# Kernel optimization log

Measured on AMD Instinct MI355X. Metric: run time of the kernel, lower is better.

The kernel has to match this reference:

```python
import jax, jax.numpy as jnp
import numpy as np

NUM_HEADS = 16

def _apply_rope(x, cos, sin):
    # x: (B, H, T, D); cos/sin: (T, D//2)
    B, H, T, D = x.shape
    xr = x.reshape(B, H, T, D // 2, 2)
    x0, x1 = xr[..., 0], xr[..., 1]
    c = cos[None, None, :, :]
    s = sin[None, None, :, :]
    out = jnp.stack([x0 * c - x1 * s, x0 * s + x1 * c], axis=-1)
    return out.reshape(B, H, T, D)


def setup_inputs() -> dict:
    key = jax.random.key(0)
    k1, k2, k3 = jax.random.split(key, 3)
    B, T, C = 2, 2048, 1024
    D = C // NUM_HEADS
    x = jax.random.normal(k1, (B, T, C), dtype=jnp.float32)
    qkv_w = jax.random.normal(k2, (3 * C, C), dtype=jnp.float32) * (C ** -0.5)
    proj_w = jax.random.normal(k3, (C, C), dtype=jnp.float32) * (C ** -0.5)
    # standard RoPE frequency table (theta = 10000)
    inv_freq = 1.0 / (10000.0 ** (jnp.arange(0, D, 2, dtype=jnp.float32) / D))  # (D/2,)
    angles = jnp.arange(T, dtype=jnp.float32)[:, None] * inv_freq[None, :]      # (T, D/2)
    return {
        "x": x,
        "freqs_cos": jnp.cos(angles),
        "freqs_sin": jnp.sin(angles),
        "qkv_w": qkv_w,
        "proj_w": proj_w,
    }


def reference(x, freqs_cos, freqs_sin, qkv_w, proj_w):
    B, T, C = x.shape
    H = NUM_HEADS
    D = C // H
    qkv = x @ qkv_w.T                                  # (B, T, 3C)
    q, k, v = jnp.split(qkv, 3, axis=-1)
    q = q.reshape(B, T, H, D).transpose(0, 2, 1, 3)    # (B, H, T, D)
    k = k.reshape(B, T, H, D).transpose(0, 2, 1, 3)
    v = v.reshape(B, T, H, D).transpose(0, 2, 1, 3)
    q = _apply_rope(q, freqs_cos, freqs_sin)
    k = _apply_rope(k, freqs_cos, freqs_sin)
    scale = 1.0 / jnp.sqrt(jnp.asarray(D, dtype=x.dtype))
    scores = jnp.einsum('bhqd,bhkd->bhqk', q, k) * scale
    causal = jnp.tril(jnp.ones((T, T), dtype=bool))
    scores = jnp.where(causal[None, None], scores, jnp.finfo(scores.dtype).min)
    attn = jax.nn.softmax(scores, axis=-1)
    out = jnp.einsum('bhqk,bhkd->bhqd', attn, v)       # (B, H, T, D)
    out = out.transpose(0, 2, 1, 3).reshape(B, T, C)
    return out @ proj_w.T
```

## Files before the change

kernel.cpp:

```cpp
#include <hip/hip_runtime.h>
#include <stdint.h>

#define DI __device__ __forceinline__

typedef unsigned short u16;
typedef __bf16 bf16x8 __attribute__((ext_vector_type(8)));
typedef unsigned short u16x8 __attribute__((ext_vector_type(8)));
typedef unsigned short u16x4 __attribute__((ext_vector_type(4)));
typedef float f32x4 __attribute__((ext_vector_type(4)));

DI u16 f2bf(float f) { __bf16 h = (__bf16)f; return __builtin_bit_cast(u16, h); }
DI float bf2f(u16 u) { return (float)__builtin_bit_cast(__bf16, u); }

DI bf16x8 ld8(const u16* p) { return __builtin_bit_cast(bf16x8, *(const u16x8*)p); }

DI f32x4 mfma16(bf16x8 a, bf16x8 b, f32x4 c) {
  return __builtin_amdgcn_mfma_f32_16x16x32_bf16(a, b, c, 0, 0, 0);
}

DI void async16(const u16* g, u16* l) {
  __builtin_amdgcn_global_load_lds((const __attribute__((address_space(1))) void*)g,
                                   (__attribute__((address_space(3))) void*)l, 16, 0, 0);
}

__global__ __launch_bounds__(256) void cast_all(const float* __restrict__ x,
                                                const float* __restrict__ qw,
                                                const float* __restrict__ pw,
                                                u16* __restrict__ xb, u16* __restrict__ qwb,
                                                u16* __restrict__ pwb) {
  const int bi = blockIdx.x;
  const float* src;
  u16* dst;
  int off;
  if (bi < 4096) {
    src = x; dst = xb; off = bi;
  } else if (bi < 7168) {
    src = qw; dst = qwb; off = bi - 4096;
  } else {
    src = pw; dst = pwb; off = bi - 7168;
  }
  const int i = off * 256 + threadIdx.x;
  const float4 v = ((const float4*)src)[i];
  u16x4 o = {f2bf(v.x), f2bf(v.y), f2bf(v.z), f2bf(v.w)};
  ((u16x4*)dst)[i] = o;
}

__global__ __launch_bounds__(256) void gemm_bt(const u16* __restrict__ A,
                                               const u16* __restrict__ W,
                                               u16* __restrict__ outp,
                                               int M, int N, int K) {
  __shared__ u16 sA[2 * 4096];
  __shared__ u16 sB[2 * 4096];
  const int tid = threadIdx.x;
  const int w = tid >> 6, L = tid & 63;
  const int lo = L & 15, quad = L >> 4;
  const int nb = N >> 7;
  const int bm = blockIdx.x / nb, bn = blockIdx.x - bm * nb;
  const int m0 = bm << 7, n0 = bn << 7;
  const int wm = (w >> 1) << 6, wn = (w & 1) << 6;

  f32x4 acc[4][4];
#pragma unroll
  for (int i = 0; i < 4; ++i)
#pragma unroll
    for (int j = 0; j < 4; ++j) acc[i][j] = 0.f;

  const int r0 = tid >> 2, s0 = tid & 3;
  const int c0 = s0 ^ ((r0 >> 1) & 3);
  const int r1 = r0 + 64;
  const int c1 = s0 ^ ((r1 >> 1) & 3);
  const u16* aP0 = A + (size_t)(m0 + r0) * K + c0 * 8;
  const u16* aP1 = A + (size_t)(m0 + r1) * K + c1 * 8;
  const u16* bP0 = W + (size_t)(n0 + r0) * K + c0 * 8;
  const u16* bP1 = W + (size_t)(n0 + r1) * K + c1 * 8;
  u16* ldA0 = &sA[tid * 8];
  u16* ldA1 = &sA[(tid + 256) * 8];
  u16* ldB0 = &sB[tid * 8];
  u16* ldB1 = &sB[(tid + 256) * 8];

  int raf[4], rbf[4];
#pragma unroll
  for (int mt = 0; mt < 4; ++mt) {
    int r = wm + mt * 16 + lo;
    raf[mt] = r * 32 + ((quad ^ ((r >> 1) & 3)) << 3);
    r = wn + mt * 16 + lo;
    rbf[mt] = r * 32 + ((quad ^ ((r >> 1) & 3)) << 3);
  }

  auto stage = [&](int buf) {
    const int bo = buf << 12;
    async16(aP0, ldA0 + bo);
    async16(aP1, ldA1 + bo);
    async16(bP0, ldB0 + bo);
    async16(bP1, ldB1 + bo);
    aP0 += 32; aP1 += 32; bP0 += 32; bP1 += 32;
  };

  const int kIters = K >> 5;
  stage(0);
  for (int kt = 0; kt < kIters; ++kt) {
    __syncthreads();
    if (kt + 1 < kIters) stage((kt + 1) & 1);
    const int bo = (kt & 1) << 12;
    bf16x8 af[4], bfr[4];
#pragma unroll
    for (int mt = 0; mt < 4; ++mt) af[mt] = ld8(&sA[bo + raf[mt]]);
#pragma unroll
    for (int nt = 0; nt < 4; ++nt) bfr[nt] = ld8(&sB[bo + rbf[nt]]);
#pragma unroll
    for (int mt = 0; mt < 4; ++mt)
#pragma unroll
      for (int nt = 0; nt < 4; ++nt)
        acc[mt][nt] = mfma16(af[mt], bfr[nt], acc[mt][nt]);
  }

#pragma unroll
  for (int mt = 0; mt < 4; ++mt) {
    const int m = m0 + wm + mt * 16 + quad * 4;
#pragma unroll
    for (int nt = 0; nt < 4; ++nt) {
      const int n = n0 + wn + nt * 16 + lo;
#pragma unroll
      for (int r = 0; r < 4; ++r) outp[(size_t)(m + r) * N + n] = f2bf(acc[mt][nt][r]);
    }
  }
}

#define QSCALE 0.18033688011112f
__global__ __launch_bounds__(256) void ropevt_k(const u16* __restrict__ qkv,
                                                const float* __restrict__ cosb,
                                                const float* __restrict__ sinb,
                                                u16* __restrict__ qo, u16* __restrict__ ko,
                                                u16* __restrict__ vto) {
  __shared__ u16 sT[64 * 64];
  const int tid = threadIdx.x;
  if (blockIdx.x < 8192) {
    const int idx = blockIdx.x * 256 + tid;
    const int i = idx & 31;
    const int t = (idx >> 5) & 2047;
    const int h = (idx >> 16) & 15;
    const int b = idx >> 20;
    const size_t src = ((size_t)(b * 2048 + t)) * 3072 + h * 64 + 2 * i;
    const float q0v = bf2f(qkv[src]), q1v = bf2f(qkv[src + 1]);
    const float k0v = bf2f(qkv[src + 1024]), k1v = bf2f(qkv[src + 1025]);
    const float c = cosb[t * 32 + i], s = sinb[t * 32 + i];
    const size_t dst = ((size_t)((b * 16 + h) * 2048 + t)) * 64 + 2 * i;
    qo[dst] = f2bf((q0v * c - q1v * s) * QSCALE);
    qo[dst + 1] = f2bf((q0v * s + q1v * c) * QSCALE);
    ko[dst] = f2bf(k0v * c - k1v * s);
    ko[dst + 1] = f2bf(k0v * s + k1v * c);
  } else {
    const int bi = blockIdx.x - 8192;
    const int bh = bi & 31;
    const int t0 = (bi >> 5) << 6;
    const int b = bh >> 4, h = bh & 15;
#pragma unroll
    for (int it = 0; it < 2; ++it) {
      const int id = tid + it * 256;
      const int tr = id >> 3, s = id & 7, c = s ^ (tr & 7);
      async16(qkv + (size_t)(b * 2048 + t0 + tr) * 3072 + 2048 + h * 64 + c * 8, &sT[id * 8]);
    }
    __syncthreads();
#pragma unroll
    for (int it = 0; it < 2; ++it) {
      const int id = tid + it * 256;
      const int d = id >> 3, ct = id & 7;
      u16x8 o;
#pragma unroll
      for (int j = 0; j < 8; ++j) {
        const int t = ct * 8 + j;
        o[j] = sT[t * 64 + (((d >> 3) ^ (t & 7)) << 3) + (d & 7)];
      }
      *(u16x8*)(vto + ((size_t)bh * 64 + d) * 2048 + t0 + ct * 8) = o;
    }
  }
}

__global__ __launch_bounds__(256) void fattn_part(const u16* __restrict__ qs,
                                                  const u16* __restrict__ ks,
                                                  const u16* __restrict__ vtb,
                                                  u16* __restrict__ opart,
                                                  float* __restrict__ lbuf) {
  __shared__ u16 sK[2 * 4096];
  __shared__ u16 sVt[2 * 4096];
  __shared__ u16 sP[4][16 * 64];
  const int tid = threadIdx.x;
  const int w = tid >> 6, L = tid & 63;
  const int lo = L & 15, quad = L >> 4;
  const int raw = blockIdx.x;
  const int part = raw & 1;
  const int bh = (raw >> 1) & 31;
  const int qi = 31 - (raw >> 6);
  const int n = qi + 1;
  const int h0 = (n + 1) >> 1;
  const int tk0 = part ? h0 : 0;
  const int tk1 = part ? n : h0;
  const size_t hoff = (size_t)bh * (2048 * 64);
  const int wq = (qi << 6) + w * 16;
  u16* sPw = sP[w];

  const int kvA = tid >> 3, cA = (tid & 7) ^ (kvA & 7);
  const int idB = tid + 256;
  const int kvB = idB >> 3, cB = (idB & 7) ^ (kvB & 7);
  const u16* kP0 = ks + hoff + (size_t)(tk0 * 64 + kvA) * 64 + cA * 8;
  const u16* kP1 = ks + hoff + (size_t)(tk0 * 64 + kvB) * 64 + cB * 8;
  const u16* vP0 = vtb + hoff + (size_t)kvA * 2048 + tk0 * 64 + cA * 8;
  const u16* vP1 = vtb + hoff + (size_t)kvB * 2048 + tk0 * 64 + cB * 8;
  u16* ldK0 = &sK[tid * 8];
  u16* ldK1 = &sK[idB * 8];
  u16* ldV0 = &sVt[tid * 8];
  u16* ldV1 = &sVt[idB * 8];

  auto stage = [&](int buf) {
    const int bo = buf << 12;
    async16(kP0, ldK0 + bo);
    async16(kP1, ldK1 + bo);
    async16(vP0, ldV0 + bo);
    async16(vP1, ldV1 + bo);
    kP0 += 4096; kP1 += 4096; vP0 += 64; vP1 += 64;
  };

  int kaOff[4][2], pOff[2], pwOff[4];
#pragma unroll
  for (int mt = 0; mt < 4; ++mt) {
    const int kv = mt * 16 + lo;
#pragma unroll
    for (int kd = 0; kd < 2; ++kd) {
      const int c = kd * 4 + quad;
      kaOff[mt][kd] = kv * 64 + ((c ^ (kv & 7)) << 3);
    }
    const int c2 = 2 * mt + (quad >> 1);
    pwOff[mt] = lo * 64 + ((c2 ^ (lo & 7)) << 3) + (quad & 1) * 4;
  }
#pragma unroll
  for (int kh = 0; kh < 2; ++kh) pOff[kh] = lo * 64 + (((kh * 4 + quad) ^ (lo & 7)) << 3);

  bf16x8 qb[2];
#pragma unroll
  for (int kd = 0; kd < 2; ++kd)
    qb[kd] = ld8(qs + hoff + (size_t)(wq + lo) * 64 + kd * 32 + quad * 8);

  bf16x8 ones;
#pragma unroll
  for (int j = 0; j < 8; ++j) ones[j] = (__bf16)1.0f;

  f32x4 lacc = 0.f;
  f32x4 ot[4];
#pragma unroll
  for (int mt = 0; mt < 4; ++mt) ot[mt] = 0.f;

  const int ntk = tk1 - tk0;
  if (ntk > 0) stage(0);
  for (int it2 = 0; it2 < ntk; ++it2) {
    __syncthreads();
    if (it2 + 1 < ntk) stage((it2 + 1) & 1);
    const int bo = (it2 & 1) << 12;
    const int kt = tk0 + it2;

    f32x4 st[4];
#pragma unroll
    for (int mt = 0; mt < 4; ++mt) st[mt] = 0.f;
#pragma unroll
    for (int mt = 0; mt < 4; ++mt)
#pragma unroll
      for (int kd = 0; kd < 2; ++kd)
        st[mt] = mfma16(ld8(&sK[bo + kaOff[mt][kd]]), qb[kd], st[mt]);

    if (kt == qi) {
      const int qg = wq + lo;
      const int kv0 = kt << 6;
#pragma unroll
      for (int mt = 0; mt < 4; ++mt)
#pragma unroll
        for (int r = 0; r < 4; ++r) {
          const int kvg = kv0 + mt * 16 + quad * 4 + r;
          if (kvg > qg) st[mt][r] = -3.0e38f;
        }
    }
#pragma unroll
    for (int mt = 0; mt < 4; ++mt) {
      u16x4 pk = {f2bf(__builtin_amdgcn_exp2f(st[mt][0])),
                  f2bf(__builtin_amdgcn_exp2f(st[mt][1])),
                  f2bf(__builtin_amdgcn_exp2f(st[mt][2])),
                  f2bf(__builtin_amdgcn_exp2f(st[mt][3]))};
      *(u16x4*)&sPw[pwOff[mt]] = pk;
    }
    asm volatile("s_waitcnt lgkmcnt(0)" ::: "memory");
    bf16x8 pbf[2];
#pragma unroll
    for (int kh = 0; kh < 2; ++kh) pbf[kh] = ld8(&sPw[pOff[kh]]);
    lacc = mfma16(ones, pbf[0], lacc);
    lacc = mfma16(ones, pbf[1], lacc);
#pragma unroll
    for (int mt = 0; mt < 4; ++mt)
#pragma unroll
      for (int kh = 0; kh < 2; ++kh)
        ot[mt] = mfma16(ld8(&sVt[bo + kaOff[mt][kh]]), pbf[kh], ot[mt]);
  }

  const int pq = bh * 32 + qi;
  u16* obase = opart + (size_t)(part * 1024 + pq) * 4096 + (size_t)(w * 16 + lo) * 64;
#pragma unroll
  for (int mt = 0; mt < 4; ++mt) {
    const int d0 = mt * 16 + quad * 4;
    u16x4 ok = {f2bf(ot[mt][0]), f2bf(ot[mt][1]), f2bf(ot[mt][2]), f2bf(ot[mt][3])};
    *(u16x4*)&obase[d0] = ok;
  }
  if (quad == 0) lbuf[(size_t)(part * 1024 + pq) * 64 + w * 16 + lo] = lacc[0];
}

__global__ __launch_bounds__(256) void gemm_merge(const u16* __restrict__ opart,
                                                  const float* __restrict__ lbuf,
                                                  const u16* __restrict__ W,
                                                  float* __restrict__ outp) {
  constexpr int N = 1024, K = 1024;
  __shared__ u16 sA[2 * 4096];
  __shared__ u16 sB[2 * 4096];
  const int tid = threadIdx.x;
  const int w = tid >> 6, L = tid & 63;
  const int lo = L & 15, quad = L >> 4;
  const int bm = blockIdx.x >> 3, bn = blockIdx.x & 7;
  const int m0 = bm << 7, n0 = bn << 7;
  const int wm = (w >> 1) << 6, wn = (w & 1) << 6;

  f32x4 acc[4][4];
#pragma unroll
  for (int i = 0; i < 4; ++i)
#pragma unroll
    for (int j = 0; j < 4; ++j) acc[i][j] = 0.f;

  const int r0 = tid >> 2, s0 = tid & 3;
  const int c0 = s0 ^ ((r0 >> 1) & 3);
  const int r1 = r0 + 64;
  const int c1 = s0 ^ ((r1 >> 1) & 3);

  const u16* bP0 = W + (size_t)(n0 + r0) * K + c0 * 8;
  const u16* bP1 = W + (size_t)(n0 + r1) * K + c1 * 8;
  u16* ldA0 = &sA[tid * 8];
  u16* ldA1 = &sA[(tid + 256) * 8];
  u16* ldB0 = &sB[tid * 8];
  u16* ldB1 = &sB[(tid + 256) * 8];

  const int m_0 = m0 + r0, m_1 = m0 + r1;
  const int pqb0 = (m_0 >> 11) * 512 + ((m_0 & 2047) >> 6);
  const int pqb1 = (m_1 >> 11) * 512 + ((m_1 & 2047) >> 6);
  const int q_0 = m_0 & 63, q_1 = m_1 & 63;
  const u16* oA0 = opart + (size_t)pqb0 * 4096 + q_0 * 64 + c0 * 8;
  const u16* oB0 = oA0 + (size_t)1024 * 4096;
  const u16* oA1 = opart + (size_t)pqb1 * 4096 + q_1 * 64 + c1 * 8;
  const u16* oB1 = oA1 + (size_t)1024 * 4096;
  const float* lq0 = lbuf + pqb0 * 64 + q_0;
  const float* lq1 = lbuf + pqb1 * 64 + q_1;

  u16x8 pr00, pr01, pr10, pr11;
  float pl0a, pl0b, pl1a, pl1b;

  auto fetchA = [&](int kt) {
    const size_t off = ((size_t)(kt >> 1) << 17) + (size_t)((kt & 1) << 5);
    pr00 = *(const u16x8*)(oA0 + off);
    pr01 = *(const u16x8*)(oB0 + off);
    pr10 = *(const u16x8*)(oA1 + off);
    pr11 = *(const u16x8*)(oB1 + off);
    if ((kt & 1) == 0) {
      const int lh = (kt >> 1) * 2048;
      pl0a = lq0[lh];
      pl0b = lq0[lh + 65536];
      pl1a = lq1[lh];
      pl1b = lq1[lh + 65536];
    }
  };
  auto commitA = [&](int buf) {
    const int bo = buf << 12;
    const float inv0 = 1.f / (pl0a + pl0b);
    const float inv1 = 1.f / (pl1a + pl1b);
    u16x8 a0, a1;
#pragma unroll
    for (int j = 0; j < 8; ++j) {
      a0[j] = f2bf((bf2f(pr00[j]) + bf2f(pr01[j])) * inv0);
      a1[j] = f2bf((bf2f(pr10[j]) + bf2f(pr11[j])) * inv1);
    }
    *(u16x8*)(ldA0 + bo) = a0;
    *(u16x8*)(ldA1 + bo) = a1;
  };
  auto stageB = [&](int buf) {
    const int bo = buf << 12;
    async16(bP0, ldB0 + bo);
    async16(bP1, ldB1 + bo);
    bP0 += 32;
    bP1 += 32;
  };

  int raf[4], rbf[4];
#pragma unroll
  for (int mt = 0; mt < 4; ++mt) {
    int r = wm + mt * 16 + lo;
    raf[mt] = r * 32 + ((quad ^ ((r >> 1) & 3)) << 3);
    r = wn + mt * 16 + lo;
    rbf[mt] = r * 32 + ((quad ^ ((r >> 1) & 3)) << 3);
  }

  stageB(0);
  fetchA(0);
  commitA(0);

  const int kIters = K >> 5;
  for (int kt = 0; kt < kIters; ++kt) {
    __syncthreads();
    if (kt + 1 < kIters) {
      stageB((kt + 1) & 1);
      fetchA(kt + 1);
    }
    const int bo = (kt & 1) << 12;
    bf16x8 af[4], bfr[4];
#pragma unroll
    for (int mt = 0; mt < 4; ++mt) af[mt] = ld8(&sA[bo + raf[mt]]);
#pragma unroll
    for (int nt = 0; nt < 4; ++nt) bfr[nt] = ld8(&sB[bo + rbf[nt]]);
#pragma unroll
    for (int mt = 0; mt < 4; ++mt)
#pragma unroll
      for (int nt = 0; nt < 4; ++nt)
        acc[mt][nt] = mfma16(af[mt], bfr[nt], acc[mt][nt]);
    if (kt + 1 < kIters) commitA((kt + 1) & 1);
  }

#pragma unroll
  for (int mt = 0; mt < 4; ++mt) {
    const int m = m0 + wm + mt * 16 + quad * 4;
#pragma unroll
    for (int nt = 0; nt < 4; ++nt) {
      const int n = n0 + wn + nt * 16 + lo;
#pragma unroll
      for (int r = 0; r < 4; ++r) outp[(size_t)(m + r) * N + n] = acc[mt][nt][r];
    }
  }
}

extern "C" void kernel_launch(void* const* d_in, const int* in_sizes, int n_in,
                              void* d_out, int out_size, void* d_ws, size_t ws_size,
                              hipStream_t stream) {
  const float* x = (const float*)d_in[0];
  const float* fcos = (const float*)d_in[1];
  const float* fsin = (const float*)d_in[2];
  const float* qkvw = (const float*)d_in[3];
  const float* projw = (const float*)d_in[4];
  float* out = (float*)d_out;

  char* ws = (char*)d_ws;
  u16* x_bf = (u16*)(ws);
  u16* qkvw_bf = (u16*)(ws + (8u << 20));
  u16* projw_bf = (u16*)(ws + (14u << 20));
  u16* qkv_bf = (u16*)(ws + (16u << 20));
  u16* q_bf = (u16*)(ws + (40u << 20));
  u16* k_bf = (u16*)(ws + (48u << 20));
  u16* vt = (u16*)(ws + (56u << 20));
  u16* opart = (u16*)(ws + (16u << 20));
  float* lbuf = (float*)(ws + (32u << 20));

  cast_all<<<8192, 256, 0, stream>>>(x, qkvw, projw, x_bf, qkvw_bf, projw_bf);
  gemm_bt<<<768, 256, 0, stream>>>(x_bf, qkvw_bf, qkv_bf, 4096, 3072, 1024);
  ropevt_k<<<9216, 256, 0, stream>>>(qkv_bf, fcos, fsin, q_bf, k_bf, vt);
  fattn_part<<<2048, 256, 0, stream>>>(q_bf, k_bf, vt, opart, lbuf);
  gemm_merge<<<256, 256, 0, stream>>>(opart, lbuf, projw_bf, out);
}
```

Baseline: 196.8 us.

## Fuse RoPE, Q scaling and V transpose into QKV GEMM epilogue

The QKV projection GEMM now applies RoPE and the softmax scale to Q and K directly in its epilogue. It stages the tile through swizzled shared memory and writes V already transposed, so the separate ropevt kernel and the intermediate qkv buffer are gone. This removes one launch and a full write plus read of the 24MB bf16 qkv tensor. In exchange the GEMM epilogue is heavier and does an extra shared-memory round trip, and the transposed V stores are 8-byte strided writes.

```diff
diff --git a/kernel.cpp b/kernel.cpp
--- a/kernel.cpp
+++ b/kernel.cpp
@@ -22,6 +22,8 @@
   __builtin_amdgcn_global_load_lds((const __attribute__((address_space(1))) void*)g,
                                    (__attribute__((address_space(3))) void*)l, 16, 0, 0);
 }
+
+#define QSCALE 0.18033688011112f
 
 __global__ __launch_bounds__(256) void cast_all(const float* __restrict__ x,
                                                 const float* __restrict__ qw,
@@ -45,17 +47,18 @@
   ((u16x4*)dst)[i] = o;
 }
 
-__global__ __launch_bounds__(256) void gemm_bt(const u16* __restrict__ A,
-                                               const u16* __restrict__ W,
-                                               u16* __restrict__ outp,
-                                               int M, int N, int K) {
-  __shared__ u16 sA[2 * 4096];
-  __shared__ u16 sB[2 * 4096];
+__global__ __launch_bounds__(256) void gemm_qkv(const u16* __restrict__ A,
+                                                const u16* __restrict__ W,
+                                                const float* __restrict__ cosb,
+                                                const float* __restrict__ sinb,
+                                                u16* __restrict__ qo, u16* __restrict__ ko,
+                                                u16* __restrict__ vto) {
+  constexpr int K = 1024;
+  __shared__ u16 smem[16384];
   const int tid = threadIdx.x;
   const int w = tid >> 6, L = tid & 63;
   const int lo = L & 15, quad = L >> 4;
-  const int nb = N >> 7;
-  const int bm = blockIdx.x / nb, bn = blockIdx.x - bm * nb;
+  const int bm = blockIdx.x / 24, bn = blockIdx.x - bm * 24;
   const int m0 = bm << 7, n0 = bn << 7;
   const int wm = (w >> 1) << 6, wn = (w & 1) << 6;
 
@@ -73,10 +76,10 @@
   const u16* aP1 = A + (size_t)(m0 + r1) * K + c1 * 8;
   const u16* bP0 = W + (size_t)(n0 + r0) * K + c0 * 8;
   const u16* bP1 = W + (size_t)(n0 + r1) * K + c1 * 8;
-  u16* ldA0 = &sA[tid * 8];
-  u16* ldA1 = &sA[(tid + 256) * 8];
-  u16* ldB0 = &sB[tid * 8];
-  u16* ldB1 = &sB[(tid + 256) * 8];
+  u16* ldA0 = &smem[tid * 8];
+  u16* ldA1 = &smem[(tid + 256) * 8];
+  u16* ldB0 = &smem[8192 + tid * 8];
+  u16* ldB1 = &smem[8192 + (tid + 256) * 8];
 
   int raf[4], rbf[4];
 #pragma unroll
@@ -84,7 +87,7 @@
     int r = wm + mt * 16 + lo;
     raf[mt] = r * 32 + ((quad ^ ((r >> 1) & 3)) << 3);
     r = wn + mt * 16 + lo;
-    rbf[mt] = r * 32 + ((quad ^ ((r >> 1) & 3)) << 3);
+    rbf[mt] = 8192 + r * 32 + ((quad ^ ((r >> 1) & 3)) << 3);
   }
 
   auto stage = [&](int buf) {
@@ -104,9 +107,9 @@
     const int bo = (kt & 1) << 12;
     bf16x8 af[4], bfr[4];
 #pragma unroll
-    for (int mt = 0; mt < 4; ++mt) af[mt] = ld8(&sA[bo + raf[mt]]);
-#pragma unroll
-    for (int nt = 0; nt < 4; ++nt) bfr[nt] = ld8(&sB[bo + rbf[nt]]);
+    for (int mt = 0; mt < 4; ++mt) af[mt] = ld8(&smem[bo + raf[mt]]);
+#pragma unroll
+    for (int nt = 0; nt < 4; ++nt) bfr[nt] = ld8(&smem[bo + rbf[nt]]);
 #pragma unroll
     for (int mt = 0; mt < 4; ++mt)
 #pragma unroll
@@ -114,64 +117,66 @@
         acc[mt][nt] = mfma16(af[mt], bfr[nt], acc[mt][nt]);
   }
 
-#pragma unroll
-  for (int mt = 0; mt < 4; ++mt) {
-    const int m = m0 + wm + mt * 16 + quad * 4;
-#pragma unroll
-    for (int nt = 0; nt < 4; ++nt) {
-      const int n = n0 + wn + nt * 16 + lo;
-#pragma unroll
-      for (int r = 0; r < 4; ++r) outp[(size_t)(m + r) * N + n] = f2bf(acc[mt][nt][r]);
-    }
-  }
-}
-
-#define QSCALE 0.18033688011112f
-__global__ __launch_bounds__(256) void ropevt_k(const u16* __restrict__ qkv,
-                                                const float* __restrict__ cosb,
-                                                const float* __restrict__ sinb,
-                                                u16* __restrict__ qo, u16* __restrict__ ko,
-                                                u16* __restrict__ vto) {
-  __shared__ u16 sT[64 * 64];
-  const int tid = threadIdx.x;
-  if (blockIdx.x < 8192) {
-    const int idx = blockIdx.x * 256 + tid;
-    const int i = idx & 31;
-    const int t = (idx >> 5) & 2047;
-    const int h = (idx >> 16) & 15;
-    const int b = idx >> 20;
-    const size_t src = ((size_t)(b * 2048 + t)) * 3072 + h * 64 + 2 * i;
-    const float q0v = bf2f(qkv[src]), q1v = bf2f(qkv[src + 1]);
-    const float k0v = bf2f(qkv[src + 1024]), k1v = bf2f(qkv[src + 1025]);
-    const float c = cosb[t * 32 + i], s = sinb[t * 32 + i];
-    const size_t dst = ((size_t)((b * 16 + h) * 2048 + t)) * 64 + 2 * i;
-    qo[dst] = f2bf((q0v * c - q1v * s) * QSCALE);
-    qo[dst + 1] = f2bf((q0v * s + q1v * c) * QSCALE);
-    ko[dst] = f2bf(k0v * c - k1v * s);
-    ko[dst + 1] = f2bf(k0v * s + k1v * c);
+  __syncthreads();
+
+  const int sec = n0 >> 10;
+  const int fbase = n0 & 1023;
+  const int b = m0 >> 11;
+  const int t0l = m0 & 2047;
+
+  if (sec == 2) {
+#pragma unroll
+    for (int mt = 0; mt < 4; ++mt) {
+      const int tb = t0l + wm + mt * 16 + quad * 4;
+#pragma unroll
+      for (int nt = 0; nt < 4; ++nt) {
+        const int f = fbase + wn + nt * 16 + lo;
+        const int h = f >> 6, d = f & 63;
+        u16x4 ok = {f2bf(acc[mt][nt][0]), f2bf(acc[mt][nt][1]), f2bf(acc[mt][nt][2]),
+                    f2bf(acc[mt][nt][3])};
+        *(u16x4*)(vto + ((size_t)((b * 16 + h) * 64 + d)) * 2048 + tb) = ok;
+      }
+    }
   } else {
-    const int bi = blockIdx.x - 8192;
-    const int bh = bi & 31;
-    const int t0 = (bi >> 5) << 6;
-    const int b = bh >> 4, h = bh & 15;
-#pragma unroll
-    for (int it = 0; it < 2; ++it) {
-      const int id = tid + it * 256;
-      const int tr = id >> 3, s = id & 7, c = s ^ (tr & 7);
-      async16(qkv + (size_t)(b * 2048 + t0 + tr) * 3072 + 2048 + h * 64 + c * 8, &sT[id * 8]);
-    }
+#pragma unroll
+    for (int mt = 0; mt < 4; ++mt)
+#pragma unroll
+      for (int nt = 0; nt < 4; ++nt) {
+        const int col = wn + nt * 16 + lo;
+#pragma unroll
+        for (int r = 0; r < 4; ++r) {
+          const int row = wm + mt * 16 + quad * 4 + r;
+          smem[row * 128 + (((col >> 3) ^ (row & 15)) << 3) + (col & 7)] =
+              f2bf(acc[mt][nt][r]);
+        }
+      }
     __syncthreads();
-#pragma unroll
-    for (int it = 0; it < 2; ++it) {
-      const int id = tid + it * 256;
-      const int d = id >> 3, ct = id & 7;
-      u16x8 o;
-#pragma unroll
-      for (int j = 0; j < 8; ++j) {
-        const int t = ct * 8 + j;
-        o[j] = sT[t * 64 + (((d >> 3) ^ (t & 7)) << 3) + (d & 7)];
+    u16* dst = (sec == 0) ? qo : ko;
+    const float scl = (sec == 0) ? QSCALE : 1.0f;
+    const int ch = tid & 7;
+    const int rr = tid >> 3;
+#pragma unroll
+    for (int pass = 0; pass < 4; ++pass) {
+      const int r = rr + pass * 32;
+      const int t = t0l + r;
+      const float4 cc = *(const float4*)&cosb[t * 32 + ch * 4];
+      const float4 ssv = *(const float4*)&sinb[t * 32 + ch * 4];
+#pragma unroll
+      for (int hh = 0; hh < 2; ++hh) {
+        const int slot = (hh * 8 + ch) ^ (r & 15);
+        u16x8 in = *(const u16x8*)&smem[r * 128 + (slot << 3)];
+        u16x8 o;
+        o[0] = f2bf((bf2f(in[0]) * cc.x - bf2f(in[1]) * ssv.x) * scl);
+        o[1] = f2bf((bf2f(in[0]) * ssv.x + bf2f(in[1]) * cc.x) * scl);
+        o[2] = f2bf((bf2f(in[2]) * cc.y - bf2f(in[3]) * ssv.y) * scl);
+        o[3] = f2bf((bf2f(in[2]) * ssv.y + bf2f(in[3]) * cc.y) * scl);
+        o[4] = f2bf((bf2f(in[4]) * cc.z - bf2f(in[5]) * ssv.z) * scl);
+        o[5] = f2bf((bf2f(in[4]) * ssv.z + bf2f(in[5]) * cc.z) * scl);
+        o[6] = f2bf((bf2f(in[6]) * cc.w - bf2f(in[7]) * ssv.w) * scl);
+        o[7] = f2bf((bf2f(in[6]) * ssv.w + bf2f(in[7]) * cc.w) * scl);
+        const int h = (fbase >> 6) + hh;
+        *(u16x8*)(dst + ((size_t)((b * 16 + h) * 2048 + t)) * 64 + ch * 8) = o;
       }
-      *(u16x8*)(vto + ((size_t)bh * 64 + d) * 2048 + t0 + ct * 8) = o;
     }
   }
 }
@@ -450,16 +455,14 @@
   u16* x_bf = (u16*)(ws);
   u16* qkvw_bf = (u16*)(ws + (8u << 20));
   u16* projw_bf = (u16*)(ws + (14u << 20));
-  u16* qkv_bf = (u16*)(ws + (16u << 20));
-  u16* q_bf = (u16*)(ws + (40u << 20));
-  u16* k_bf = (u16*)(ws + (48u << 20));
-  u16* vt = (u16*)(ws + (56u << 20));
-  u16* opart = (u16*)(ws + (16u << 20));
-  float* lbuf = (float*)(ws + (32u << 20));
+  u16* q_bf = (u16*)(ws + (16u << 20));
+  u16* k_bf = (u16*)(ws + (24u << 20));
+  u16* vt = (u16*)(ws + (32u << 20));
+  u16* opart = (u16*)(ws + (40u << 20));
+  float* lbuf = (float*)(ws + (56u << 20));
 
   cast_all<<<8192, 256, 0, stream>>>(x, qkvw, projw, x_bf, qkvw_bf, projw_bf);
-  gemm_bt<<<768, 256, 0, stream>>>(x_bf, qkvw_bf, qkv_bf, 4096, 3072, 1024);
-  ropevt_k<<<9216, 256, 0, stream>>>(qkv_bf, fcos, fsin, q_bf, k_bf, vt);
+  gemm_qkv<<<768, 256, 0, stream>>>(x_bf, qkvw_bf, fcos, fsin, q_bf, k_bf, vt);
   fattn_part<<<2048, 256, 0, stream>>>(q_bf, k_bf, vt, opart, lbuf);
   gemm_merge<<<256, 256, 0, stream>>>(opart, lbuf, projw_bf, out);
 }
```

Result: no change. 197.6 us (+0.4%).
